# Performance work log

Measured on AMD Instinct MI355X. Metric: run time of the kernel, lower is better.

## Reference

```python
import jax, jax.numpy as jnp
import numpy as np

C = 512       # out_channels
RATIO = 2
K = C // RATIO          # init_channels = 256
NEW = K * (RATIO - 1)   # new_channels = 256
H = W = 160
EPS = 1e-5


def _conv(x, w, pad, groups=1):
    return jax.lax.conv_general_dilated(
        x, w, (1, 1), [(pad, pad), (pad, pad)],
        dimension_numbers=("NCHW", "OIHW", "NCHW"),
        feature_group_count=groups)


def _bn(x, g, b, m, v):
    scale = (g / jnp.sqrt(v + EPS))[None, :, None, None]
    return (x - m[None, :, None, None]) * scale + b[None, :, None, None]


def setup_inputs() -> dict:
    key = jax.random.key(0)
    ks = jax.random.split(key, 16)
    s = 0.05
    return {
        "x": jax.random.normal(ks[0], (1, C, H, W), jnp.float32),
        "w_fc1": jax.random.normal(ks[1], (K, C), jnp.float32) * s,
        "w_fc2": jax.random.normal(ks[2], (C, K), jnp.float32) * s,
        "w_cheap": jax.random.normal(ks[3], (NEW, 1, 3, 3), jnp.float32) * s,  # depthwise, groups=K
        "bn1_g": jnp.ones((NEW,), jnp.float32),
        "bn1_b": jnp.zeros((NEW,), jnp.float32),
        "bn1_m": jax.random.normal(ks[4], (NEW,), jnp.float32) * s,
        "bn1_v": jax.random.uniform(ks[5], (NEW,), jnp.float32, 0.5, 1.5),
        "w_dc1": jax.random.normal(ks[6], (C, 2 * C, 1, 1), jnp.float32) * s,
        "b_dc1": jax.random.normal(ks[7], (C,), jnp.float32) * s,
        "bn2_g": jnp.ones((C,), jnp.float32),
        "bn2_b": jnp.zeros((C,), jnp.float32),
        "bn2_m": jax.random.normal(ks[8], (C,), jnp.float32) * s,
        "bn2_v": jax.random.uniform(ks[9], (C,), jnp.float32, 0.5, 1.5),
        "w_dc2": jax.random.normal(ks[10], (C, C, 3, 3), jnp.float32) * s,
        "b_dc2": jax.random.normal(ks[11], (C,), jnp.float32) * s,
    }


def reference(x, w_fc1, w_fc2, w_cheap, bn1_g, bn1_b, bn1_m, bn1_v,
              w_dc1, b_dc1, bn2_g, bn2_b, bn2_m, bn2_v, w_dc2, b_dc2):
    # ---- channel attention (CBAM-style shared MLP over avg+max pool) ----
    avg = x.mean(axis=(2, 3))                      # [1, C]
    mx = x.max(axis=(2, 3))                        # [1, C]
    mlp = lambda p: jax.nn.relu(p @ w_fc1.T) @ w_fc2.T
    scales = jax.nn.sigmoid(mlp(avg) + mlp(mx))    # [1, C]
    # ---- sort-based top-K channel select, kept in channel-index order ----
    # torch: sort desc, drop channels ranked >= K via boolean mask (mask is in
    # channel-index order), equivalent to gathering sorted top-K indices.
    _, top_idx = jax.lax.top_k(scales[0], K)
    idx = jnp.sort(top_idx)
    x1 = x[:, idx]                                 # [1, K, H, W]
    # ---- cheap operation: depthwise 3x3 + BN + ReLU ----
    x2 = jax.nn.relu(_bn(_conv(x1, w_cheap, 1, groups=K), bn1_g, bn1_b, bn1_m, bn1_v))
    # ---- concat [x*scales, x1, x2] -> 2C channels ----
    cat = jnp.concatenate([x * scales[:, :, None, None], x1, x2], axis=1)
    # ---- down_channel: 1x1 conv + BN + 3x3 conv + ReLU ----
    h = _conv(cat, w_dc1, 0) + b_dc1[None, :, None, None]
    h = _bn(h, bn2_g, bn2_b, bn2_m, bn2_v)
    h = _conv(h, w_dc2, 1) + b_dc2[None, :, None, None]
    return jax.nn.relu(h)
```

## Files before the change

kernel.cpp:

```cpp
#include <hip/hip_runtime.h>
#include <math.h>

#define C 512
#define K 256
#define HW 160
#define NPIX (HW*HW)
#define PW 162
#define EPS 1e-5f

typedef __attribute__((ext_vector_type(8))) short s16x8;
typedef __attribute__((ext_vector_type(16))) float f32x16;

__device__ __forceinline__ unsigned short f2bf(float f) {
    unsigned int u = __float_as_uint(f);
    u += 0x7fffu + ((u >> 16) & 1u);
    return (unsigned short)(u >> 16);
}

__device__ __forceinline__ void ldg_lds16(const void* g, void* l) {
    __builtin_amdgcn_global_load_lds((const __attribute__((address_space(1))) unsigned int*)g,
                                     (__attribute__((address_space(3))) unsigned int*)l, 16, 0, 0);
}

__global__ void reduce_kernel(const float* __restrict__ x,
                              float* __restrict__ avg, float* __restrict__ mx) {
    int c = blockIdx.x;
    const float* xc = x + (size_t)c * NPIX;
    float s = 0.f, m = -INFINITY;
    for (int p = threadIdx.x; p < NPIX; p += 256) {
        float v = xc[p];
        s += v;
        m = fmaxf(m, v);
    }
    __shared__ float ss[256], sm[256];
    ss[threadIdx.x] = s; sm[threadIdx.x] = m;
    __syncthreads();
    for (int o = 128; o > 0; o >>= 1) {
        if (threadIdx.x < o) {
            ss[threadIdx.x] += ss[threadIdx.x + o];
            sm[threadIdx.x] = fmaxf(sm[threadIdx.x], sm[threadIdx.x + o]);
        }
        __syncthreads();
    }
    if (threadIdx.x == 0) {
        avg[c] = ss[0] / (float)NPIX;
        mx[c]  = sm[0];
    }
}

__global__ void mlp_select_kernel(const float* __restrict__ avg,
                                  const float* __restrict__ mx,
                                  const float* __restrict__ w_fc1,
                                  const float* __restrict__ w_fc2,
                                  float* __restrict__ scales_out,
                                  int* __restrict__ idx,
                                  int* __restrict__ pos) {
    __shared__ float s_avg[C], s_mx[C], s_h[K], s_scales[C];
    __shared__ int s_sel[C];
    int t = threadIdx.x;
    s_avg[t] = avg[t];
    s_mx[t]  = mx[t];
    __syncthreads();
    if (t < K) {
        float ha = 0.f, hm = 0.f;
        const float4* wr = (const float4*)(w_fc1 + (size_t)t * C);
        for (int c = 0; c < C / 4; c++) {
            float4 w = wr[c];
            ha += s_avg[4*c]*w.x + s_avg[4*c+1]*w.y + s_avg[4*c+2]*w.z + s_avg[4*c+3]*w.w;
            hm += s_mx[4*c]*w.x + s_mx[4*c+1]*w.y + s_mx[4*c+2]*w.z + s_mx[4*c+3]*w.w;
        }
        s_h[t] = fmaxf(ha, 0.f) + fmaxf(hm, 0.f);
    }
    __syncthreads();
    {
        float o = 0.f;
        const float4* wr = (const float4*)(w_fc2 + (size_t)t * K);
        for (int k = 0; k < K / 4; k++) {
            float4 w = wr[k];
            o += s_h[4*k]*w.x + s_h[4*k+1]*w.y + s_h[4*k+2]*w.z + s_h[4*k+3]*w.w;
        }
        float sc = 1.f / (1.f + expf(-o));
        s_scales[t] = sc;
        scales_out[t] = sc;
    }
    __syncthreads();
    {
        float v = s_scales[t];
        int rank = 0;
        for (int i = 0; i < C; i++) {
            float u = s_scales[i];
            rank += (u > v) || (u == v && i < t);
        }
        s_sel[t] = (rank < K) ? 1 : 0;
    }
    __syncthreads();
    {
        int p = 0;
        for (int i = 0; i < t; i++) p += s_sel[i];
        if (s_sel[t]) { idx[p] = t; pos[t] = p; }
        else pos[t] = -1;
    }
}

__global__ void affine_kernel(const float* __restrict__ b_dc1,
                              const float* __restrict__ g2, const float* __restrict__ b2,
                              const float* __restrict__ m2, const float* __restrict__ v2,
                              float* __restrict__ scale2, float* __restrict__ shift2) {
    int c = threadIdx.x;
    float s = g2[c] * rsqrtf(v2[c] + EPS);
    scale2[c] = s;
    shift2[c] = (b_dc1[c] - m2[c]) * s + b2[c];
}

__global__ void wa_bf16_kernel(const float* __restrict__ w_dc1,
                               const float* __restrict__ scales,
                               const int* __restrict__ pos,
                               unsigned short* __restrict__ wA) {
    int co = blockIdx.x;
    const float* wr = w_dc1 + (size_t)co * 1024;
    for (int c = threadIdx.x; c < 768; c += 256) {
        float v;
        if (c < 512) {
            v = wr[c] * scales[c];
            int pp = pos[c];
            if (pp >= 0) v += wr[512 + pp];
        } else {
            v = wr[768 + (c - 512)];
        }
        wA[(size_t)co * 768 + c] = f2bf(v);
    }
}

__global__ void w3_kernel(const float* __restrict__ w_dc2, unsigned short* __restrict__ w3) {
    int co = blockIdx.x, t = blockIdx.y;
    for (int ci = threadIdx.x; ci < 512; ci += 256) {
        w3[((size_t)t * 512 + co) * 512 + ci] = f2bf(w_dc2[((size_t)co * 512 + ci) * 9 + t]);
    }
}

__global__ void dw_kernel(const float* __restrict__ x,
                          const int* __restrict__ idx,
                          const float* __restrict__ wch,
                          const float* __restrict__ g1,
                          const float* __restrict__ b1,
                          const float* __restrict__ m1,
                          const float* __restrict__ v1,
                          float* __restrict__ x2) {
    int k = blockIdx.y;
    int p = blockIdx.x * 256 + threadIdx.x;
    int c = idx[k];
    int y = p / HW, xx = p % HW;
    const float* xc = x + (size_t)c * NPIX;
    const float* wk = wch + k * 9;
    float acc = 0.f;
#pragma unroll
    for (int dy = 0; dy < 3; dy++) {
        int yy = y + dy - 1;
        if (yy < 0 || yy >= HW) continue;
#pragma unroll
        for (int dx = 0; dx < 3; dx++) {
            int xv = xx + dx - 1;
            if (xv < 0 || xv >= HW) continue;
            acc += xc[yy * HW + xv] * wk[dy * 3 + dx];
        }
    }
    float s = g1[k] * rsqrtf(v1[k] + EPS);
    float t = (acc - m1[k]) * s + b1[k];
    x2[(size_t)k * NPIX + p] = fmaxf(t, 0.f);
}

__global__ void transpose_kernel(const float* __restrict__ x, const float* __restrict__ x2,
                                 unsigned short* __restrict__ xcat) {
    __shared__ float tile[32][33];
    int tx = threadIdx.x & 31, ty = threadIdx.x >> 5;
    int pbase = blockIdx.x * 32, cbase = blockIdx.y * 32;
#pragma unroll
    for (int j = 0; j < 4; j++) {
        int c = cbase + ty + j * 8;
        float v = (c < 512) ? x[(size_t)c * NPIX + pbase + tx]
                            : x2[(size_t)(c - 512) * NPIX + pbase + tx];
        tile[ty + j * 8][tx] = v;
    }
    __syncthreads();
#pragma unroll
    for (int j = 0; j < 4; j++) {
        int p = pbase + ty + j * 8;
        xcat[(size_t)p * 768 + cbase + tx] = f2bf(tile[tx][ty + j * 8]);
    }
}

__global__ void zero_border(unsigned short* __restrict__ hpad) {
    int t = blockIdx.x * 256 + threadIdx.x;
    int pix = t >> 6;
    int pos;
    if (pix < 162)      pos = pix;
    else if (pix < 324) pos = 161 * PW + (pix - 162);
    else {
        int r = pix - 324;
        pos = (1 + (r >> 1)) * PW + ((r & 1) ? 161 : 0);
    }
    *(uint4*)&hpad[(size_t)pos * 512 + (t & 63) * 8] = make_uint4(0u, 0u, 0u, 0u);
}

__global__ __launch_bounds__(128, 2) void conv1_mfma(const unsigned short* __restrict__ xcat,
        const unsigned short* __restrict__ wA,
        const float* __restrict__ scale2, const float* __restrict__ shift2,
        unsigned short* __restrict__ hpad) {
    __shared__ unsigned short Al[2][640 * 8];
    __shared__ unsigned short Bl[2][512 * 8];
    int y = blockIdx.x, co0 = blockIdx.y * 128;
    int tid = threadIdx.x, lane = tid & 63, wv = tid >> 6;
    int l31 = lane & 31, q = lane >> 5;
    f32x16 acc[5][2] = {};
    int svA = tid >> 2, sjA = tid & 3;
    int sgA = sjA ^ ((svA >> 1) & 3);

    const unsigned short* arow = xcat + ((size_t)y * HW) * 768;
    const unsigned short* brow = wA + (size_t)co0 * 768;

    {
#pragma unroll
        for (int r = 0; r < 5; r++)
            ldg_lds16(arow + (size_t)(r * 32 + svA) * 768 + sgA * 8, &Al[0][(r * 128 + wv * 64) * 8]);
#pragma unroll
        for (int r = 0; r < 4; r++)
            ldg_lds16(brow + (size_t)(r * 32 + svA) * 768 + sgA * 8, &Bl[0][(r * 128 + wv * 64) * 8]);
    }
    __syncthreads();
    for (int ph = 0; ph < 24; ph++) {
        int p = ph & 1;
        if (ph < 23) {
            int kc = (ph + 1) * 32;
#pragma unroll
            for (int r = 0; r < 5; r++)
                ldg_lds16(arow + (size_t)(r * 32 + svA) * 768 + kc + sgA * 8,
                          &Al[p ^ 1][(r * 128 + wv * 64) * 8]);
#pragma unroll
            for (int r = 0; r < 4; r++)
                ldg_lds16(brow + (size_t)(r * 32 + svA) * 768 + kc + sgA * 8,
                          &Bl[p ^ 1][(r * 128 + wv * 64) * 8]);
        }
#pragma unroll
        for (int s = 0; s < 2; s++) {
            int g0 = s * 2 + q;
            s16x8 bf[2], af[5];
            const char* bbase = (const char*)Bl[p] + wv * 4096 + l31 * 64 + ((g0 ^ ((l31 >> 1) & 3)) << 4);
#pragma unroll
            for (int j = 0; j < 2; j++) bf[j] = *(const s16x8*)(bbase + j * 2048);
            const char* abase = (const char*)Al[p] + l31 * 64 + ((g0 ^ ((l31 >> 1) & 3)) << 4);
#pragma unroll
            for (int i = 0; i < 5; i++) af[i] = *(const s16x8*)(abase + i * 2048);
#pragma unroll
            for (int i = 0; i < 5; i++)
#pragma unroll
                for (int j = 0; j < 2; j++)
                    acc[i][j] = __builtin_amdgcn_mfma_f32_32x32x16_bf16(af[i], bf[j], acc[i][j], 0, 0, 0);
        }
        __syncthreads();
    }
#pragma unroll
    for (int j = 0; j < 2; j++) {
        int co = co0 + wv * 64 + j * 32 + l31;
        float s2 = scale2[co], sh = shift2[co];
#pragma unroll
        for (int i = 0; i < 5; i++) {
#pragma unroll
            for (int rg = 0; rg < 4; rg++) {
#pragma unroll
                for (int t = 0; t < 4; t++) {
                    int px = i * 32 + t + rg * 8 + q * 4;
                    size_t pp = (size_t)(y + 1) * PW + px + 1;
                    hpad[pp * 512 + co] = f2bf(acc[i][j][rg * 4 + t] * s2 + sh);
                }
            }
        }
    }
}

__global__ __launch_bounds__(128, 2) void conv3_mfma(const unsigned short* __restrict__ hpad,
        const unsigned short* __restrict__ w3,
        const float* __restrict__ bias, float* __restrict__ out) {
    __shared__ unsigned short Al[2][648 * 8];
    __shared__ unsigned short Bl[2][1536 * 8];
    int y = blockIdx.x, co0 = blockIdx.y * 128;
    int tid = threadIdx.x, lane = tid & 63, wv = tid >> 6;
    int l31 = lane & 31, q = lane >> 5;
    f32x16 acc[5][2] = {};
    int svA = tid >> 2, sjA = tid & 3;
    int sgA = sjA ^ ((svA >> 1) & 3);

    auto stage = [&](int ph, int buf) {
        int dy = ph >> 4, kc = (ph & 15) * 32;
        const unsigned short* ab = hpad + ((size_t)(y + dy) * PW) * 512 + kc;
#pragma unroll
        for (int r = 0; r < 6; r++) {
            int gi = r * 128 + tid;
            if (gi < 648)
                ldg_lds16(ab + (size_t)(r * 32 + svA) * 512 + sgA * 8,
                          &Al[buf][(r * 128 + wv * 64) * 8]);
        }
        const unsigned short* bb = w3 + ((size_t)(dy * 3) * 512 + co0) * 512 + kc;
#pragma unroll
        for (int r = 0; r < 12; r++) {
            int tt = r >> 2, co = (r & 3) * 32 + svA;
            ldg_lds16(bb + ((size_t)tt * 512 + co) * 512 + sgA * 8,
                      &Bl[buf][(r * 128 + wv * 64) * 8]);
        }
    };

    stage(0, 0);
    __syncthreads();
    for (int ph = 0; ph < 48; ph++) {
        int p = ph & 1;
        if (ph < 47) stage(ph + 1, p ^ 1);
#pragma unroll
        for (int dx = 0; dx < 3; dx++) {
#pragma unroll
            for (int s = 0; s < 2; s++) {
                int g0 = s * 2 + q;
                s16x8 bf[2], af[5];
                const char* bbase = (const char*)Bl[p] + dx * 8192 + wv * 4096 + l31 * 64
                                    + ((g0 ^ ((l31 >> 1) & 3)) << 4);
#pragma unroll
                for (int j = 0; j < 2; j++) bf[j] = *(const s16x8*)(bbase + j * 2048);
                int pl = dx + l31;
                const char* abase = (const char*)Al[p] + pl * 64
                                    + ((g0 ^ ((pl >> 1) & 3)) << 4);
#pragma unroll
                for (int i = 0; i < 5; i++) af[i] = *(const s16x8*)(abase + i * 2048);
#pragma unroll
                for (int i = 0; i < 5; i++)
#pragma unroll
                    for (int j = 0; j < 2; j++)
                        acc[i][j] = __builtin_amdgcn_mfma_f32_32x32x16_bf16(af[i], bf[j], acc[i][j], 0, 0, 0);
            }
        }
        __syncthreads();
    }
#pragma unroll
    for (int j = 0; j < 2; j++) {
        int co = co0 + wv * 64 + j * 32 + l31;
        float b = bias[co];
        float* op = out + (size_t)co * NPIX + y * HW;
#pragma unroll
        for (int i = 0; i < 5; i++) {
#pragma unroll
            for (int rg = 0; rg < 4; rg++) {
                int px = i * 32 + rg * 8 + q * 4;
                float4 v;
                v.x = fmaxf(acc[i][j][rg * 4 + 0] + b, 0.f);
                v.y = fmaxf(acc[i][j][rg * 4 + 1] + b, 0.f);
                v.z = fmaxf(acc[i][j][rg * 4 + 2] + b, 0.f);
                v.w = fmaxf(acc[i][j][rg * 4 + 3] + b, 0.f);
                *(float4*)&op[px] = v;
            }
        }
    }
}

extern "C" void kernel_launch(void* const* d_in, const int* in_sizes, int n_in,
                              void* d_out, int out_size, void* d_ws, size_t ws_size,
                              hipStream_t stream) {
    const float* x      = (const float*)d_in[0];
    const float* w_fc1  = (const float*)d_in[1];
    const float* w_fc2  = (const float*)d_in[2];
    const float* w_ch   = (const float*)d_in[3];
    const float* bn1_g  = (const float*)d_in[4];
    const float* bn1_b  = (const float*)d_in[5];
    const float* bn1_m  = (const float*)d_in[6];
    const float* bn1_v  = (const float*)d_in[7];
    const float* w_dc1  = (const float*)d_in[8];
    const float* b_dc1  = (const float*)d_in[9];
    const float* bn2_g  = (const float*)d_in[10];
    const float* bn2_b  = (const float*)d_in[11];
    const float* bn2_m  = (const float*)d_in[12];
    const float* bn2_v  = (const float*)d_in[13];
    const float* w_dc2  = (const float*)d_in[14];
    const float* b_dc2  = (const float*)d_in[15];
    float* out = (float*)d_out;

    char* ws = (char*)d_ws;
    float* avg    = (float*)(ws + 0);
    float* mx     = (float*)(ws + 2048);
    float* scales = (float*)(ws + 4096);
    int*   idx    = (int*)  (ws + 6144);
    int*   pos    = (int*)  (ws + 7168);
    float* scale2 = (float*)(ws + 9216);
    float* shift2 = (float*)(ws + 11264);
    unsigned short* wA   = (unsigned short*)(ws + 16384);
    unsigned short* w3   = (unsigned short*)(ws + 802816);
    float*          x2   = (float*)         (ws + 5521408);
    unsigned short* xcat = (unsigned short*)(ws + 31735808);
    unsigned short* hpad = (unsigned short*)(ws + 71057408);

    reduce_kernel<<<C, 256, 0, stream>>>(x, avg, mx);
    mlp_select_kernel<<<1, C, 0, stream>>>(avg, mx, w_fc1, w_fc2, scales, idx, pos);
    affine_kernel<<<1, C, 0, stream>>>(b_dc1, bn2_g, bn2_b, bn2_m, bn2_v, scale2, shift2);
    wa_bf16_kernel<<<C, 256, 0, stream>>>(w_dc1, scales, pos, wA);
    w3_kernel<<<dim3(C, 9), 256, 0, stream>>>(w_dc2, w3);
    zero_border<<<161, 256, 0, stream>>>(hpad);
    dw_kernel<<<dim3(NPIX / 256, K), 256, 0, stream>>>(x, idx, w_ch, bn1_g, bn1_b, bn1_m, bn1_v, x2);
    transpose_kernel<<<dim3(NPIX / 32, 24), 256, 0, stream>>>(x, x2, xcat);
    conv1_mfma<<<dim3(HW, 4), 128, 0, stream>>>(xcat, wA, scale2, shift2, hpad);
    conv3_mfma<<<dim3(HW, 4), 128, 0, stream>>>(hpad, w3, b_dc2, out);
}
```

Baseline: 533.8 us.

## Merge prep kernels, fuse depthwise into transpose, single-wave MFMA conv blocks

Combines the weight conversion, border zeroing and BN affine setup into one prep kernel, and fuses the depthwise conv with the bf16 transpose write so the x2 intermediate is never materialised. The reduce kernel now uses float4 loads. Both MFMA convolutions become one-wave blocks with 64 output channels, precomputed offsets and vmcnt/lgkmcnt waits in place of __syncthreads, with LDS fragments loaded before the next prefetch is issued. This cuts launches and memory traffic but halves the output-channel reuse per block and relies on hand-placed waitcnts for correctness.

```diff
diff --git a/kernel.cpp b/kernel.cpp
--- a/kernel.cpp
+++ b/kernel.cpp
@@ -22,15 +22,18 @@
                                      (__attribute__((address_space(3))) unsigned int*)l, 16, 0, 0);
 }
 
+#define WAIT_VM0()  asm volatile("s_waitcnt vmcnt(0)" ::: "memory")
+#define WAIT_LGKM0() asm volatile("s_waitcnt lgkmcnt(0)" ::: "memory")
+
 __global__ void reduce_kernel(const float* __restrict__ x,
                               float* __restrict__ avg, float* __restrict__ mx) {
     int c = blockIdx.x;
-    const float* xc = x + (size_t)c * NPIX;
+    const float4* xc = (const float4*)(x + (size_t)c * NPIX);
     float s = 0.f, m = -INFINITY;
-    for (int p = threadIdx.x; p < NPIX; p += 256) {
-        float v = xc[p];
-        s += v;
-        m = fmaxf(m, v);
+    for (int p = threadIdx.x; p < NPIX / 4; p += 256) {
+        float4 v = xc[p];
+        s += v.x + v.y + v.z + v.w;
+        m = fmaxf(m, fmaxf(fmaxf(v.x, v.y), fmaxf(v.z, v.w)));
     }
     __shared__ float ss[256], sm[256];
     ss[threadIdx.x] = s; sm[threadIdx.x] = m;
@@ -102,74 +105,94 @@
     }
 }
 
-__global__ void affine_kernel(const float* __restrict__ b_dc1,
-                              const float* __restrict__ g2, const float* __restrict__ b2,
-                              const float* __restrict__ m2, const float* __restrict__ v2,
-                              float* __restrict__ scale2, float* __restrict__ shift2) {
-    int c = threadIdx.x;
-    float s = g2[c] * rsqrtf(v2[c] + EPS);
-    scale2[c] = s;
-    shift2[c] = (b_dc1[c] - m2[c]) * s + b2[c];
-}
-
-__global__ void wa_bf16_kernel(const float* __restrict__ w_dc1,
-                               const float* __restrict__ scales,
-                               const int* __restrict__ pos,
-                               unsigned short* __restrict__ wA) {
-    int co = blockIdx.x;
-    const float* wr = w_dc1 + (size_t)co * 1024;
-    for (int c = threadIdx.x; c < 768; c += 256) {
-        float v;
-        if (c < 512) {
-            v = wr[c] * scales[c];
-            int pp = pos[c];
-            if (pp >= 0) v += wr[512 + pp];
-        } else {
-            v = wr[768 + (c - 512)];
-        }
-        wA[(size_t)co * 768 + c] = f2bf(v);
-    }
-}
-
-__global__ void w3_kernel(const float* __restrict__ w_dc2, unsigned short* __restrict__ w3) {
-    int co = blockIdx.x, t = blockIdx.y;
-    for (int ci = threadIdx.x; ci < 512; ci += 256) {
-        w3[((size_t)t * 512 + co) * 512 + ci] = f2bf(w_dc2[((size_t)co * 512 + ci) * 9 + t]);
-    }
-}
-
-__global__ void dw_kernel(const float* __restrict__ x,
-                          const int* __restrict__ idx,
-                          const float* __restrict__ wch,
-                          const float* __restrict__ g1,
-                          const float* __restrict__ b1,
-                          const float* __restrict__ m1,
-                          const float* __restrict__ v1,
-                          float* __restrict__ x2) {
-    int k = blockIdx.y;
-    int p = blockIdx.x * 256 + threadIdx.x;
-    int c = idx[k];
-    int y = p / HW, xx = p % HW;
-    const float* xc = x + (size_t)c * NPIX;
-    const float* wk = wch + k * 9;
-    float acc = 0.f;
-#pragma unroll
-    for (int dy = 0; dy < 3; dy++) {
-        int yy = y + dy - 1;
-        if (yy < 0 || yy >= HW) continue;
-#pragma unroll
-        for (int dx = 0; dx < 3; dx++) {
-            int xv = xx + dx - 1;
-            if (xv < 0 || xv >= HW) continue;
-            acc += xc[yy * HW + xv] * wk[dy * 3 + dx];
-        }
-    }
-    float s = g1[k] * rsqrtf(v1[k] + EPS);
-    float t = (acc - m1[k]) * s + b1[k];
-    x2[(size_t)k * NPIX + p] = fmaxf(t, 0.f);
-}
-
-__global__ void transpose_kernel(const float* __restrict__ x, const float* __restrict__ x2,
+__global__ void prep_kernel(const float* __restrict__ w_dc2, unsigned short* __restrict__ w3,
+                            const float* __restrict__ w_dc1, const float* __restrict__ scales,
+                            const int* __restrict__ pos, unsigned short* __restrict__ wA,
+                            unsigned short* __restrict__ hpad,
+                            const float* __restrict__ b_dc1,
+                            const float* __restrict__ g2, const float* __restrict__ b2,
+                            const float* __restrict__ m2, const float* __restrict__ v2,
+                            float* __restrict__ scale2, float* __restrict__ shift2) {
+    int b = blockIdx.x;
+    if (b < 4608) {
+        int t = b >> 9, co = b & 511;
+        for (int ci = threadIdx.x; ci < 512; ci += 256)
+            w3[((size_t)t * 512 + co) * 512 + ci] = f2bf(w_dc2[((size_t)co * 512 + ci) * 9 + t]);
+    } else if (b < 5120) {
+        int co = b - 4608;
+        const float* wr = w_dc1 + (size_t)co * 1024;
+        for (int c = threadIdx.x; c < 768; c += 256) {
+            float v;
+            if (c < 512) {
+                v = wr[c] * scales[c];
+                int pp = pos[c];
+                if (pp >= 0) v += wr[512 + pp];
+            } else {
+                v = wr[768 + (c - 512)];
+            }
+            wA[(size_t)co * 768 + c] = f2bf(v);
+        }
+    } else if (b < 5281) {
+        int t = (b - 5120) * 256 + threadIdx.x;
+        int pix = t >> 6;
+        int p;
+        if (pix < 162)      p = pix;
+        else if (pix < 324) p = 161 * PW + (pix - 162);
+        else {
+            int r = pix - 324;
+            p = (1 + (r >> 1)) * PW + ((r & 1) ? 161 : 0);
+        }
+        *(uint4*)&hpad[(size_t)p * 512 + (t & 63) * 8] = make_uint4(0u, 0u, 0u, 0u);
+    } else {
+        for (int c = threadIdx.x; c < C; c += 256) {
+            float s = g2[c] * rsqrtf(v2[c] + EPS);
+            scale2[c] = s;
+            shift2[c] = (b_dc1[c] - m2[c]) * s + b2[c];
+        }
+    }
+}
+
+__global__ void dw_t_kernel(const float* __restrict__ x,
+                            const int* __restrict__ idx,
+                            const float* __restrict__ wch,
+                            const float* __restrict__ g1, const float* __restrict__ b1,
+                            const float* __restrict__ m1, const float* __restrict__ v1,
+                            unsigned short* __restrict__ xcat) {
+    __shared__ float tile[32][33];
+    int tx = threadIdx.x & 31, ty = threadIdx.x >> 5;
+    int pbase = blockIdx.x * 32, kbase = blockIdx.y * 32;
+    int y = pbase / HW, x0 = pbase % HW;
+    int px = x0 + tx;
+#pragma unroll
+    for (int jj = 0; jj < 4; jj++) {
+        int k = kbase + ty + jj * 8;
+        int c = idx[k];
+        const float* xc = x + (size_t)c * NPIX;
+        const float* wk = wch + k * 9;
+        float acc = 0.f;
+#pragma unroll
+        for (int dy = 0; dy < 3; dy++) {
+            int yy = y + dy - 1;
+            if (yy < 0 || yy >= HW) continue;
+#pragma unroll
+            for (int dx = 0; dx < 3; dx++) {
+                int xv = px + dx - 1;
+                if (xv < 0 || xv >= HW) continue;
+                acc += xc[yy * HW + xv] * wk[dy * 3 + dx];
+            }
+        }
+        float s = g1[k] * rsqrtf(v1[k] + EPS);
+        tile[ty + jj * 8][tx] = fmaxf((acc - m1[k]) * s + b1[k], 0.f);
+    }
+    __syncthreads();
+#pragma unroll
+    for (int jj = 0; jj < 4; jj++) {
+        int p = pbase + ty + jj * 8;
+        xcat[(size_t)p * 768 + 512 + kbase + tx] = f2bf(tile[tx][ty + jj * 8]);
+    }
+}
+
+__global__ void transpose_kernel(const float* __restrict__ x,
                                  unsigned short* __restrict__ xcat) {
     __shared__ float tile[32][33];
     int tx = threadIdx.x & 31, ty = threadIdx.x >> 5;
@@ -177,9 +200,7 @@
 #pragma unroll
     for (int j = 0; j < 4; j++) {
         int c = cbase + ty + j * 8;
-        float v = (c < 512) ? x[(size_t)c * NPIX + pbase + tx]
-                            : x2[(size_t)(c - 512) * NPIX + pbase + tx];
-        tile[ty + j * 8][tx] = v;
+        tile[ty + j * 8][tx] = x[(size_t)c * NPIX + pbase + tx];
     }
     __syncthreads();
 #pragma unroll
@@ -189,78 +210,77 @@
     }
 }
 
-__global__ void zero_border(unsigned short* __restrict__ hpad) {
-    int t = blockIdx.x * 256 + threadIdx.x;
-    int pix = t >> 6;
-    int pos;
-    if (pix < 162)      pos = pix;
-    else if (pix < 324) pos = 161 * PW + (pix - 162);
-    else {
-        int r = pix - 324;
-        pos = (1 + (r >> 1)) * PW + ((r & 1) ? 161 : 0);
-    }
-    *(uint4*)&hpad[(size_t)pos * 512 + (t & 63) * 8] = make_uint4(0u, 0u, 0u, 0u);
-}
-
-__global__ __launch_bounds__(128, 2) void conv1_mfma(const unsigned short* __restrict__ xcat,
+__global__ __launch_bounds__(64, 1) void conv1_mfma(const unsigned short* __restrict__ xcat,
         const unsigned short* __restrict__ wA,
         const float* __restrict__ scale2, const float* __restrict__ shift2,
         unsigned short* __restrict__ hpad) {
     __shared__ unsigned short Al[2][640 * 8];
-    __shared__ unsigned short Bl[2][512 * 8];
-    int y = blockIdx.x, co0 = blockIdx.y * 128;
-    int tid = threadIdx.x, lane = tid & 63, wv = tid >> 6;
+    __shared__ unsigned short Bl[2][256 * 8];
+    int y = blockIdx.x, co0 = blockIdx.y * 64;
+    int lane = threadIdx.x;
     int l31 = lane & 31, q = lane >> 5;
     f32x16 acc[5][2] = {};
-    int svA = tid >> 2, sjA = tid & 3;
-    int sgA = sjA ^ ((svA >> 1) & 3);
-
-    const unsigned short* arow = xcat + ((size_t)y * HW) * 768;
+
+    int aoff[10], boff[4];
+#pragma unroll
+    for (int r = 0; r < 10; r++) {
+        int g = r * 64 + lane;
+        int px = g >> 2, jg = (g & 3) ^ ((px >> 1) & 3);
+        aoff[r] = px * 768 + jg * 8;
+    }
+#pragma unroll
+    for (int r = 0; r < 4; r++) {
+        int g = r * 64 + lane;
+        int co = g >> 2, jg = (g & 3) ^ ((co >> 1) & 3);
+        boff[r] = co * 768 + jg * 8;
+    }
+    int raoff[2];
+#pragma unroll
+    for (int s = 0; s < 2; s++)
+        raoff[s] = l31 * 64 + (((s * 2 + q) ^ ((l31 >> 1) & 3)) << 4);
+    const unsigned short* arow = xcat + (size_t)y * HW * 768;
     const unsigned short* brow = wA + (size_t)co0 * 768;
 
-    {
-#pragma unroll
-        for (int r = 0; r < 5; r++)
-            ldg_lds16(arow + (size_t)(r * 32 + svA) * 768 + sgA * 8, &Al[0][(r * 128 + wv * 64) * 8]);
-#pragma unroll
-        for (int r = 0; r < 4; r++)
-            ldg_lds16(brow + (size_t)(r * 32 + svA) * 768 + sgA * 8, &Bl[0][(r * 128 + wv * 64) * 8]);
-    }
-    __syncthreads();
+#pragma unroll
+    for (int r = 0; r < 10; r++) ldg_lds16(arow + aoff[r], &Al[0][r * 512]);
+#pragma unroll
+    for (int r = 0; r < 4; r++)  ldg_lds16(brow + boff[r], &Bl[0][r * 512]);
+
     for (int ph = 0; ph < 24; ph++) {
-        int p = ph & 1;
+        const unsigned short* Ar = Al[ph & 1];
+        const unsigned short* Br = Bl[ph & 1];
+        WAIT_VM0();
+        s16x8 af[5][2], bf[2][2];
+#pragma unroll
+        for (int s = 0; s < 2; s++) {
+#pragma unroll
+            for (int i = 0; i < 5; i++)
+                af[i][s] = *(const s16x8*)((const char*)Ar + i * 2048 + raoff[s]);
+#pragma unroll
+            for (int j = 0; j < 2; j++)
+                bf[j][s] = *(const s16x8*)((const char*)Br + j * 2048 + raoff[s]);
+        }
+        WAIT_LGKM0();
         if (ph < 23) {
             int kc = (ph + 1) * 32;
-#pragma unroll
-            for (int r = 0; r < 5; r++)
-                ldg_lds16(arow + (size_t)(r * 32 + svA) * 768 + kc + sgA * 8,
-                          &Al[p ^ 1][(r * 128 + wv * 64) * 8]);
-#pragma unroll
-            for (int r = 0; r < 4; r++)
-                ldg_lds16(brow + (size_t)(r * 32 + svA) * 768 + kc + sgA * 8,
-                          &Bl[p ^ 1][(r * 128 + wv * 64) * 8]);
-        }
-#pragma unroll
-        for (int s = 0; s < 2; s++) {
-            int g0 = s * 2 + q;
-            s16x8 bf[2], af[5];
-            const char* bbase = (const char*)Bl[p] + wv * 4096 + l31 * 64 + ((g0 ^ ((l31 >> 1) & 3)) << 4);
-#pragma unroll
-            for (int j = 0; j < 2; j++) bf[j] = *(const s16x8*)(bbase + j * 2048);
-            const char* abase = (const char*)Al[p] + l31 * 64 + ((g0 ^ ((l31 >> 1) & 3)) << 4);
-#pragma unroll
-            for (int i = 0; i < 5; i++) af[i] = *(const s16x8*)(abase + i * 2048);
+            unsigned short* An = Al[(ph + 1) & 1];
+            unsigned short* Bn = Bl[(ph + 1) & 1];
+#pragma unroll
+            for (int r = 0; r < 10; r++) ldg_lds16(arow + kc + aoff[r], &An[r * 512]);
+#pragma unroll
+            for (int r = 0; r < 4; r++)  ldg_lds16(brow + kc + boff[r], &Bn[r * 512]);
+        }
+#pragma unroll
+        for (int s = 0; s < 2; s++)
 #pragma unroll
             for (int i = 0; i < 5; i++)
 #pragma unroll
                 for (int j = 0; j < 2; j++)
-                    acc[i][j] = __builtin_amdgcn_mfma_f32_32x32x16_bf16(af[i], bf[j], acc[i][j], 0, 0, 0);
-        }
-        __syncthreads();
+                    acc[i][j] = __builtin_amdgcn_mfma_f32_32x32x16_bf16(af[i][s], bf[j][s], acc[i][j], 0, 0, 0);
     }
 #pragma unroll
     for (int j = 0; j < 2; j++) {
-        int co = co0 + wv * 64 + j * 32 + l31;
+        int co = co0 + j * 32 + l31;
         float s2 = scale2[co], sh = shift2[co];
 #pragma unroll
         for (int i = 0; i < 5; i++) {
@@ -277,69 +297,87 @@
     }
 }
 
-__global__ __launch_bounds__(128, 2) void conv3_mfma(const unsigned short* __restrict__ hpad,
+__global__ __launch_bounds__(64, 1) void conv3_mfma(const unsigned short* __restrict__ hpad,
         const unsigned short* __restrict__ w3,
         const float* __restrict__ bias, float* __restrict__ out) {
     __shared__ unsigned short Al[2][648 * 8];
-    __shared__ unsigned short Bl[2][1536 * 8];
-    int y = blockIdx.x, co0 = blockIdx.y * 128;
-    int tid = threadIdx.x, lane = tid & 63, wv = tid >> 6;
+    __shared__ unsigned short Bl[2][768 * 8];
+    int y = blockIdx.x, co0 = blockIdx.y * 64;
+    int lane = threadIdx.x;
     int l31 = lane & 31, q = lane >> 5;
     f32x16 acc[5][2] = {};
-    int svA = tid >> 2, sjA = tid & 3;
-    int sgA = sjA ^ ((svA >> 1) & 3);
+
+    int aoff[11], boff[12];
+#pragma unroll
+    for (int r = 0; r < 11; r++) {
+        int g = r * 64 + lane;
+        int px = g >> 2, jg = (g & 3) ^ ((px >> 1) & 3);
+        aoff[r] = px * 512 + jg * 8;
+    }
+#pragma unroll
+    for (int r = 0; r < 12; r++) {
+        int g = r * 64 + lane;
+        int tt = g >> 8, co = (g >> 2) & 63, jg = (g & 3) ^ ((co >> 1) & 3);
+        boff[r] = (tt * 512 + co) * 512 + jg * 8;
+    }
+    int raoff[3][2], rboff[2];
+#pragma unroll
+    for (int dx = 0; dx < 3; dx++)
+#pragma unroll
+        for (int s = 0; s < 2; s++) {
+            int m = l31 + dx;
+            raoff[dx][s] = m * 64 + ((((s * 2 + q)) ^ ((m >> 1) & 3)) << 4);
+        }
+#pragma unroll
+    for (int s = 0; s < 2; s++)
+        rboff[s] = l31 * 64 + (((s * 2 + q) ^ ((l31 >> 1) & 3)) << 4);
 
     auto stage = [&](int ph, int buf) {
         int dy = ph >> 4, kc = (ph & 15) * 32;
         const unsigned short* ab = hpad + ((size_t)(y + dy) * PW) * 512 + kc;
-#pragma unroll
-        for (int r = 0; r < 6; r++) {
-            int gi = r * 128 + tid;
-            if (gi < 648)
-                ldg_lds16(ab + (size_t)(r * 32 + svA) * 512 + sgA * 8,
-                          &Al[buf][(r * 128 + wv * 64) * 8]);
-        }
+        unsigned short* An = Al[buf];
+#pragma unroll
+        for (int r = 0; r < 10; r++) ldg_lds16(ab + aoff[r], &An[r * 512]);
+        if (lane < 8)                ldg_lds16(ab + aoff[10], &An[10 * 512]);
         const unsigned short* bb = w3 + ((size_t)(dy * 3) * 512 + co0) * 512 + kc;
-#pragma unroll
-        for (int r = 0; r < 12; r++) {
-            int tt = r >> 2, co = (r & 3) * 32 + svA;
-            ldg_lds16(bb + ((size_t)tt * 512 + co) * 512 + sgA * 8,
-                      &Bl[buf][(r * 128 + wv * 64) * 8]);
-        }
+        unsigned short* Bn = Bl[buf];
+#pragma unroll
+        for (int r = 0; r < 12; r++) ldg_lds16(bb + boff[r], &Bn[r * 512]);
     };
 
     stage(0, 0);
-    __syncthreads();
     for (int ph = 0; ph < 48; ph++) {
-        int p = ph & 1;
-        if (ph < 47) stage(ph + 1, p ^ 1);
+        const unsigned short* Ar = Al[ph & 1];
+        const unsigned short* Br = Bl[ph & 1];
+        WAIT_VM0();
+        s16x8 af[3][5][2], bf[3][2][2];
 #pragma unroll
         for (int dx = 0; dx < 3; dx++) {
 #pragma unroll
             for (int s = 0; s < 2; s++) {
-                int g0 = s * 2 + q;
-                s16x8 bf[2], af[5];
-                const char* bbase = (const char*)Bl[p] + dx * 8192 + wv * 4096 + l31 * 64
-                                    + ((g0 ^ ((l31 >> 1) & 3)) << 4);
-#pragma unroll
-                for (int j = 0; j < 2; j++) bf[j] = *(const s16x8*)(bbase + j * 2048);
-                int pl = dx + l31;
-                const char* abase = (const char*)Al[p] + pl * 64
-                                    + ((g0 ^ ((pl >> 1) & 3)) << 4);
-#pragma unroll
-                for (int i = 0; i < 5; i++) af[i] = *(const s16x8*)(abase + i * 2048);
 #pragma unroll
                 for (int i = 0; i < 5; i++)
+                    af[dx][i][s] = *(const s16x8*)((const char*)Ar + i * 2048 + raoff[dx][s]);
+#pragma unroll
+                for (int j = 0; j < 2; j++)
+                    bf[dx][j][s] = *(const s16x8*)((const char*)Br + dx * 4096 + j * 2048 + rboff[s]);
+            }
+        }
+        WAIT_LGKM0();
+        if (ph < 47) stage(ph + 1, (ph + 1) & 1);
+#pragma unroll
+        for (int dx = 0; dx < 3; dx++)
+#pragma unroll
+            for (int s = 0; s < 2; s++)
+#pragma unroll
+                for (int i = 0; i < 5; i++)
 #pragma unroll
                     for (int j = 0; j < 2; j++)
-                        acc[i][j] = __builtin_amdgcn_mfma_f32_32x32x16_bf16(af[i], bf[j], acc[i][j], 0, 0, 0);
-            }
-        }
-        __syncthreads();
+                        acc[i][j] = __builtin_amdgcn_mfma_f32_32x32x16_bf16(af[dx][i][s], bf[dx][j][s], acc[i][j], 0, 0, 0);
     }
 #pragma unroll
     for (int j = 0; j < 2; j++) {
-        int co = co0 + wv * 64 + j * 32 + l31;
+        int co = co0 + j * 32 + l31;
         float b = bias[co];
         float* op = out + (size_t)co * NPIX + y * HW;
 #pragma unroll
@@ -389,18 +427,15 @@
     float* shift2 = (float*)(ws + 11264);
     unsigned short* wA   = (unsigned short*)(ws + 16384);
     unsigned short* w3   = (unsigned short*)(ws + 802816);
-    float*          x2   = (float*)         (ws + 5521408);
     unsigned short* xcat = (unsigned short*)(ws + 31735808);
     unsigned short* hpad = (unsigned short*)(ws + 71057408);
 
     reduce_kernel<<<C, 256, 0, stream>>>(x, avg, mx);
     mlp_select_kernel<<<1, C, 0, stream>>>(avg, mx, w_fc1, w_fc2, scales, idx, pos);
-    affine_kernel<<<1, C, 0, stream>>>(b_dc1, bn2_g, bn2_b, bn2_m, bn2_v, scale2, shift2);
-    wa_bf16_kernel<<<C, 256, 0, stream>>>(w_dc1, scales, pos, wA);
-    w3_kernel<<<dim3(C, 9), 256, 0, stream>>>(w_dc2, w3);
-    zero_border<<<161, 256, 0, stream>>>(hpad);
-    dw_kernel<<<dim3(NPIX / 256, K), 256, 0, stream>>>(x, idx, w_ch, bn1_g, bn1_b, bn1_m, bn1_v, x2);
-    transpose_kernel<<<dim3(NPIX / 32, 24), 256, 0, stream>>>(x, x2, xcat);
-    conv1_mfma<<<dim3(HW, 4), 128, 0, stream>>>(xcat, wA, scale2, shift2, hpad);
-    conv3_mfma<<<dim3(HW, 4), 128, 0, stream>>>(hpad, w3, b_dc2, out);
-}
+    prep_kernel<<<5282, 256, 0, stream>>>(w_dc2, w3, w_dc1, scales, pos, wA, hpad,
+                                          b_dc1, bn2_g, bn2_b, bn2_m, bn2_v, scale2, shift2);
+    dw_t_kernel<<<dim3(800, 8), 256, 0, stream>>>(x, idx, w_ch, bn1_g, bn1_b, bn1_m, bn1_v, xcat);
+    transpose_kernel<<<dim3(800, 16), 256, 0, stream>>>(x, xcat);
+    conv1_mfma<<<dim3(HW, 8), 64, 0, stream>>>(xcat, wA, scale2, shift2, hpad);
+    conv3_mfma<<<dim3(HW, 8), 64, 0, stream>>>(hpad, w3, b_dc2, out);
+}
```

Result: faster. 451.5 us (-15.4%).
